# Performance work log

Hardware: AMD Instinct MI355X
Metric: run time of the kernel (lower is better)

Reference implementation:

```python
import jax, jax.numpy as jnp
import numpy as np

B = 32768
IN_DIM = 256
HIDDEN = 256  # max(64, in_dim)
E = 8         # num_size_classes
K = 5         # num_depth_classes


def setup_inputs() -> dict:
    key = jax.random.key(0)
    ks = jax.random.split(key, 6)
    x = jax.random.normal(ks[0], (B, IN_DIM), dtype=jnp.float32)
    size_idx = jax.random.randint(ks[1], (B,), 0, E, dtype=jnp.int32)
    s1 = 1.0 / np.sqrt(IN_DIM)
    s2 = 1.0 / np.sqrt(HIDDEN)
    W1 = jax.random.uniform(ks[2], (E, IN_DIM, HIDDEN), jnp.float32, -s1, s1)
    b1 = jax.random.uniform(ks[3], (E, HIDDEN), jnp.float32, -s1, s1)
    W2 = jax.random.uniform(ks[4], (E, HIDDEN, K - 1), jnp.float32, -s2, s2)
    b2 = jax.random.uniform(ks[5], (E, K - 1), jnp.float32, -s2, s2)
    return {"x": x, "size_idx": size_idx, "W1": W1, "b1": b1, "W2": W2, "b2": b2}


def ordinal_logits_to_probs(logits):
    # logits: [B, K-1] cumulative ordinal logits -> [B, K] class probabilities
    q = jax.nn.sigmoid(logits)
    probs = jnp.concatenate(
        [1.0 - q[:, :1], q[:, :-1] - q[:, 1:], q[:, -1:]], axis=1)
    probs = jnp.clip(probs, 1e-8)
    return probs / jnp.clip(jnp.sum(probs, axis=1, keepdims=True), 1e-8)


def reference(x, size_idx, W1, b1, W2, b2):
    # Hard expert dispatch: each sample routed to expert[size_idx].
    # Equivalent to torch's boolean-mask loop (every row has a valid expert).
    # Compute all experts densely (grouped GEMM), then select per sample.
    h = jax.nn.relu(jnp.einsum('bi,eih->beh', x, W1) + b1)       # [B,E,H]
    logits_all = jnp.einsum('beh,ehk->bek', h, W2) + b2           # [B,E,K-1]
    idx = size_idx.astype(jnp.int32)[:, None, None]               # [B,1,1]
    logits = jnp.take_along_axis(logits_all, idx, axis=1)[:, 0]   # [B,K-1]
    probs = ordinal_logits_to_probs(logits)
    return logits, probs
```

## Files before the change

### kernel.cpp

```cpp
#include <hip/hip_runtime.h>
#include <stdint.h>
#include <math.h>

#define B_N   32768
#define INDIM 256
#define HID   256
#define NE    8
#define KM1   4
#define KCLS  5
#define BM    64
#define CAP   8192
#define TPE   (CAP / BM)
#define NBLK  (NE * TPE)

typedef __bf16 bf16x8 __attribute__((ext_vector_type(8)));
typedef float  f32x4  __attribute__((ext_vector_type(4)));
typedef unsigned short u16x8 __attribute__((ext_vector_type(8)));

__device__ __forceinline__ unsigned short f2bf(float f) {
    union { float f; unsigned u; } v; v.f = f;
    unsigned r = v.u + 0x7FFFu + ((v.u >> 16) & 1u);
    return (unsigned short)(r >> 16);
}
__device__ __forceinline__ float bf2f(unsigned short b) {
    union { unsigned u; float f; } v; v.u = ((unsigned)b) << 16;
    return v.f;
}
__device__ __forceinline__ int SWZ(int r, int c) { return c ^ (r & 7); }

__device__ __forceinline__ void gload_lds16(const void* g, void* l) {
    __builtin_amdgcn_global_load_lds(
        (__attribute__((address_space(1))) unsigned int*)(g),
        (__attribute__((address_space(3))) unsigned int*)(l),
        16, 0, 0);
}

__global__ __launch_bounds__(256) void k_w1t(const float* __restrict__ W1,
                                             const int* __restrict__ sidx,
                                             unsigned short* __restrict__ w1p,
                                             int* __restrict__ part) {
    __shared__ float tile[64][65];
    __shared__ int wc[4][NE];
    int t    = threadIdx.x;
    int b    = blockIdx.x;
    int lane = t & 63;
    int wave = t >> 6;

    int es = sidx[b * 256 + t];
    #pragma unroll
    for (int t2 = 0; t2 < NE; ++t2) {
        unsigned long long m = __ballot(es == t2);
        if (lane == t2) wc[wave][t2] = (int)__popcll(m);
    }

    int e  = b >> 4, ti = (b >> 2) & 3, th = b & 3;
    const float* src = W1 + (((size_t)e * INDIM) + (size_t)ti * 64) * HID + th * 64;
    int col = t & 63, r0 = (t >> 6) * 16;
    #pragma unroll
    for (int rr = 0; rr < 16; ++rr)
        tile[r0 + rr][col] = src[(size_t)(r0 + rr) * HID + col];
    __syncthreads();

    if (t < NE) {
        part[(2 * b) * NE + t]     = wc[0][t] + wc[1][t];
        part[(2 * b + 1) * NE + t] = wc[2][t] + wc[3][t];
    }

    int u = t >> 6;
    #pragma unroll
    for (int ks2 = 0; ks2 < 2; ++ks2) {
        int ks = ti * 2 + ks2, nb = th * 4 + u;
        u16x8 v;
        #pragma unroll
        for (int j = 0; j < 8; ++j)
            v[j] = f2bf(tile[ks2 * 32 + (lane >> 4) * 8 + j][u * 16 + (lane & 15)]);
        *(u16x8*)&w1p[((((size_t)e * 8 + ks) * 16 + nb) * 64 + lane) * 8] = v;
    }
}

__global__ __launch_bounds__(256) void k_xscat(
    const float* __restrict__ x, const int* __restrict__ sidx,
    const int* __restrict__ part,
    unsigned short* __restrict__ xb, int* __restrict__ perm,
    int* __restrict__ meta)
{
    __shared__ int pp[256][NE];
    __shared__ int pr[8][NE][2];
    __shared__ int pre8[NE], tot8[NE];
    __shared__ int wc0[NE];
    __shared__ int posbuf[128];

    int t    = threadIdx.x;
    int b    = blockIdx.x;
    int lane = t & 63;
    int wave = t >> 6;

    #pragma unroll
    for (int e2 = 0; e2 < NE; ++e2) pp[t][e2] = part[t * NE + e2];

    int e_own = 0, posw = 0;
    if (t < 128) {
        e_own = sidx[b * 128 + t];
        #pragma unroll
        for (int t2 = 0; t2 < NE; ++t2) {
            unsigned long long m = __ballot(e_own == t2);
            if (e_own == t2) posw = (int)__popcll(m & ((1ull << lane) - 1ull));
            if (wave == 0 && lane == t2) wc0[t2] = (int)__popcll(m);
        }
    }
    __syncthreads();

    if (t < 64) {
        int e2 = t & 7, r = t >> 3;
        int sb = 0, sa = 0;
        #pragma unroll
        for (int c = 0; c < 32; ++c) {
            int ch = r * 32 + c;
            int v  = pp[ch][e2];
            sb += (ch < b) ? v : 0;
            sa += v;
        }
        pr[r][e2][0] = sb; pr[r][e2][1] = sa;
    }
    __syncthreads();
    if (t < NE) {
        int sb = 0, sa = 0;
        #pragma unroll
        for (int r = 0; r < 8; ++r) { sb += pr[r][t][0]; sa += pr[r][t][1]; }
        pre8[t] = sb; tot8[t] = sa;
        meta[t] = sa;
    }
    __syncthreads();

    if (t < 128) {
        int rank = pre8[e_own] + ((wave == 1) ? wc0[e_own] : 0) + posw;
        int pos  = e_own * CAP + rank;
        posbuf[t] = pos;
        perm[pos] = b * 128 + t;
    }
    __syncthreads();

    {
        int si  = t & 127, h = t >> 7;
        int pos = posbuf[si];
        int r   = pos & (BM - 1);
        const float* xr = x + (size_t)(b * 128 + si) * INDIM + h * 128;
        unsigned short* dst = xb + (size_t)pos * 256;
        #pragma unroll
        for (int cc = 0; cc < 16; ++cc) {
            int ch   = h * 16 + cc;
            int slot = SWZ(r, ch);
            f32x4 a0 = *(const f32x4*)(xr + cc * 8);
            f32x4 a1 = *(const f32x4*)(xr + cc * 8 + 4);
            u16x8 v;
            v[0] = f2bf(a0[0]); v[1] = f2bf(a0[1]); v[2] = f2bf(a0[2]); v[3] = f2bf(a0[3]);
            v[4] = f2bf(a1[0]); v[5] = f2bf(a1[1]); v[6] = f2bf(a1[2]); v[7] = f2bf(a1[3]);
            *(u16x8*)&dst[slot * 8] = v;
        }
    }
}

__global__ __launch_bounds__(256, 4) void k_main(
    const float* __restrict__ b1, const float* __restrict__ W2,
    const float* __restrict__ b2,
    const unsigned short* __restrict__ w1p,
    const unsigned short* __restrict__ xb,
    const int* __restrict__ perm, const int* __restrict__ meta,
    float* __restrict__ out)
{
    __shared__ unsigned short xs[BM * 256];
    __shared__ float w2s[1040];

    int bid = (blockIdx.x & 7) * TPE + (blockIdx.x >> 3);
    int e   = bid >> 7;
    int tl  = bid & (TPE - 1);
    int cnt = meta[e];
    int rb  = tl * BM;
    if (rb >= cnt) return;
    int segc = cnt - rb;

    int tid  = threadIdx.x;
    int lane = tid & 63;
    int wave = tid >> 6;
    int r15  = lane & 15;
    int hi   = lane >> 4;

    const unsigned short* xbt = xb + ((size_t)e * CAP + rb) * 256;
    #pragma unroll
    for (int it = 0; it < 8; ++it)
        gload_lds16(xbt + ((size_t)it * 256 + tid) * 8, &xs[it * 2048 + wave * 512]);

    const unsigned short* w1pe = w1p + (size_t)e * (8 * 16 * 64 * 8);
    auto loadB = [&](int ks, int ni) -> bf16x8 {
        return *(const bf16x8*)&w1pe[(((ks * 16 + wave * 4 + ni) * 64) + lane) * 8];
    };
    bf16x8 bcur[4];
    #pragma unroll
    for (int ni = 0; ni < 4; ++ni) bcur[ni] = loadB(0, ni);

    {
        const float* w2e = W2 + (size_t)e * HID * KM1;
        f32x4 wv = *(const f32x4*)(w2e + (size_t)tid * 4);
        *(f32x4*)&w2s[tid * 4 + (tid >> 6) * 4] = wv;
    }
    __syncthreads();

    f32x4 acc[4][4];
    #pragma unroll
    for (int mi = 0; mi < 4; ++mi)
        #pragma unroll
        for (int ni = 0; ni < 4; ++ni) {
            f32x4 z = {0.f, 0.f, 0.f, 0.f};
            acc[mi][ni] = z;
        }

    #pragma unroll
    for (int ks = 0; ks < 8; ++ks) {
        bf16x8 bnext[4];
        if (ks < 7) {
            #pragma unroll
            for (int ni = 0; ni < 4; ++ni) bnext[ni] = loadB(ks + 1, ni);
        }
        bf16x8 af[4];
        #pragma unroll
        for (int mi = 0; mi < 4; ++mi) {
            int r = mi * 16 + r15;
            af[mi] = *(const bf16x8*)&xs[r * 256 + (SWZ(r, ks * 4 + hi) << 3)];
        }
        #pragma unroll
        for (int mi = 0; mi < 4; ++mi)
            #pragma unroll
            for (int ni = 0; ni < 4; ++ni)
                acc[mi][ni] = __builtin_amdgcn_mfma_f32_16x16x32_bf16(
                    af[mi], bcur[ni], acc[mi][ni], 0, 0, 0);
        if (ks < 7) {
            #pragma unroll
            for (int ni = 0; ni < 4; ++ni) bcur[ni] = bnext[ni];
        }
    }
    __syncthreads();

    float b1v[4];
    #pragma unroll
    for (int ni = 0; ni < 4; ++ni)
        b1v[ni] = b1[e * HID + wave * 64 + ni * 16 + r15];
    #pragma unroll
    for (int mi = 0; mi < 4; ++mi) {
        #pragma unroll
        for (int ni = 0; ni < 4; ++ni) {
            int colg  = wave * 64 + ni * 16 + r15;
            int chunk = colg >> 3;
            #pragma unroll
            for (int j = 0; j < 4; ++j) {
                int rowg = mi * 16 + hi * 4 + j;
                float h = fmaxf(acc[mi][ni][j] + b1v[ni], 0.f);
                xs[rowg * 256 + (SWZ(rowg, chunk) << 3) + (colg & 7)] = f2bf(h);
            }
        }
    }
    __syncthreads();

    int row = tid >> 2;
    int q   = tid & 3;
    f32x4 lac = {0.f, 0.f, 0.f, 0.f};
    #pragma unroll
    for (int s = 0; s < 8; ++s) {
        int c = q * 8 + s;
        u16x8 hv = *(const u16x8*)&xs[row * 256 + (SWZ(row, c) << 3)];
        #pragma unroll
        for (int j = 0; j < 8; ++j) {
            int k = c * 8 + j;
            float hf = bf2f(hv[j]);
            const f32x4 wv = *(const f32x4*)&w2s[k * 4 + (k >> 6) * 4];
            lac[0] += hf * wv[0]; lac[1] += hf * wv[1];
            lac[2] += hf * wv[2]; lac[3] += hf * wv[3];
        }
    }
    #pragma unroll
    for (int c4 = 0; c4 < 4; ++c4) {
        lac[c4] += __shfl_xor(lac[c4], 1, 4);
        lac[c4] += __shfl_xor(lac[c4], 2, 4);
    }

    if (row < segc) {
        int smp = perm[(size_t)e * CAP + rb + row];
        const float* b2e = b2 + e * KM1;
        float l0 = lac[0] + b2e[0], l1 = lac[1] + b2e[1];
        float l2 = lac[2] + b2e[2], l3 = lac[3] + b2e[3];
        float q0 = 1.f / (1.f + expf(-l0)), q1 = 1.f / (1.f + expf(-l1));
        float q2v = 1.f / (1.f + expf(-l2)), q3 = 1.f / (1.f + expf(-l3));
        float p0 = fmaxf(1.f - q0, 1e-8f), p1 = fmaxf(q0 - q1, 1e-8f);
        float p2 = fmaxf(q1 - q2v, 1e-8f), p3 = fmaxf(q2v - q3, 1e-8f);
        float p4 = fmaxf(q3, 1e-8f);
        float inv = 1.f / (p0 + p1 + p2 + p3 + p4);
        float myl = (q & 1) ? ((q & 2) ? l3 : l1) : ((q & 2) ? l2 : l0);
        float myp = (q & 1) ? ((q & 2) ? p3 : p1) : ((q & 2) ? p2 : p0);
        out[(size_t)smp * KM1 + q] = myl;
        float* probs = out + (size_t)B_N * KM1;
        probs[(size_t)smp * KCLS + q] = myp * inv;
        if (q == 3) probs[(size_t)smp * KCLS + 4] = p4 * inv;
    }
}

extern "C" void kernel_launch(void* const* d_in, const int* in_sizes, int n_in,
                              void* d_out, int out_size, void* d_ws, size_t ws_size,
                              hipStream_t stream) {
    const float* x   = (const float*)d_in[0];
    const int*   sid = (const int*)d_in[1];
    const float* W1  = (const float*)d_in[2];
    const float* b1  = (const float*)d_in[3];
    const float* W2  = (const float*)d_in[4];
    const float* b2  = (const float*)d_in[5];
    float* out = (float*)d_out;

    char* ws = (char*)d_ws;
    unsigned short* w1p = (unsigned short*)ws;
    unsigned short* xb  = (unsigned short*)(ws + 1048576);
    int* perm = (int*)(ws + 1048576 + 33554432);
    int* part = (int*)(ws + 1048576 + 33554432 + 262144);
    int* meta = (int*)(ws + 1048576 + 33554432 + 262144 + 8192);

    k_w1t  <<<dim3(128),  dim3(256), 0, stream>>>(W1, sid, w1p, part);
    k_xscat<<<dim3(256),  dim3(256), 0, stream>>>(x, sid, part, xb, perm, meta);
    k_main <<<dim3(NBLK), dim3(256), 0, stream>>>(b1, W2, b2, w1p, xb, perm, meta, out);
}
```

Measured before the change: 42.19 us.

## Split scatter kernel into rank computation and wide x-to-bf16 conversion kernel

Splits the combined rank-and-scatter kernel into two kernels. k_rank computes each sample's destination position and writes it to a new pos buffer. k_xconv then converts x to bf16 and scatters it using 2048 blocks, with 16 threads per row, instead of 256 blocks where each thread walked half a row. The aim is more parallelism and memory-level concurrency for the bandwidth-bound conversion. It also transposes the shared partition array to cut LDS bank conflicts. The cost is an extra kernel launch and a round trip of the pos buffer through global memory.

```diff
diff --git a/kernel.cpp b/kernel.cpp
--- a/kernel.cpp
+++ b/kernel.cpp
@@ -78,17 +78,13 @@
     }
 }
 
-__global__ __launch_bounds__(256) void k_xscat(
-    const float* __restrict__ x, const int* __restrict__ sidx,
-    const int* __restrict__ part,
-    unsigned short* __restrict__ xb, int* __restrict__ perm,
-    int* __restrict__ meta)
+__global__ __launch_bounds__(256) void k_rank(
+    const int* __restrict__ sidx, const int* __restrict__ part,
+    int* __restrict__ pos, int* __restrict__ perm, int* __restrict__ meta)
 {
-    __shared__ int pp[256][NE];
+    __shared__ int pp[NE][260];
     __shared__ int pr[8][NE][2];
-    __shared__ int pre8[NE], tot8[NE];
-    __shared__ int wc0[NE];
-    __shared__ int posbuf[128];
+    __shared__ int pre8[NE], tot8[NE], wc0[NE];
 
     int t    = threadIdx.x;
     int b    = blockIdx.x;
@@ -96,7 +92,7 @@
     int wave = t >> 6;
 
     #pragma unroll
-    for (int e2 = 0; e2 < NE; ++e2) pp[t][e2] = part[t * NE + e2];
+    for (int e2 = 0; e2 < NE; ++e2) pp[e2][t] = part[t * NE + e2];
 
     int e_own = 0, posw = 0;
     if (t < 128) {
@@ -116,7 +112,7 @@
         #pragma unroll
         for (int c = 0; c < 32; ++c) {
             int ch = r * 32 + c;
-            int v  = pp[ch][e2];
+            int v  = pp[e2][ch];
             sb += (ch < b) ? v : 0;
             sa += v;
         }
@@ -134,29 +130,33 @@
 
     if (t < 128) {
         int rank = pre8[e_own] + ((wave == 1) ? wc0[e_own] : 0) + posw;
-        int pos  = e_own * CAP + rank;
-        posbuf[t] = pos;
-        perm[pos] = b * 128 + t;
-    }
-    __syncthreads();
-
-    {
-        int si  = t & 127, h = t >> 7;
-        int pos = posbuf[si];
-        int r   = pos & (BM - 1);
-        const float* xr = x + (size_t)(b * 128 + si) * INDIM + h * 128;
-        unsigned short* dst = xb + (size_t)pos * 256;
-        #pragma unroll
-        for (int cc = 0; cc < 16; ++cc) {
-            int ch   = h * 16 + cc;
-            int slot = SWZ(r, ch);
-            f32x4 a0 = *(const f32x4*)(xr + cc * 8);
-            f32x4 a1 = *(const f32x4*)(xr + cc * 8 + 4);
-            u16x8 v;
-            v[0] = f2bf(a0[0]); v[1] = f2bf(a0[1]); v[2] = f2bf(a0[2]); v[3] = f2bf(a0[3]);
-            v[4] = f2bf(a1[0]); v[5] = f2bf(a1[1]); v[6] = f2bf(a1[2]); v[7] = f2bf(a1[3]);
-            *(u16x8*)&dst[slot * 8] = v;
-        }
+        int p    = e_own * CAP + rank;
+        pos[b * 128 + t] = p;
+        perm[p] = b * 128 + t;
+    }
+}
+
+__global__ __launch_bounds__(256) void k_xconv(
+    const float* __restrict__ x, const int* __restrict__ pos,
+    unsigned short* __restrict__ xb)
+{
+    int g    = blockIdx.x;
+    int rloc = threadIdx.x >> 4;
+    int p    = threadIdx.x & 15;
+    int smp  = g * 16 + rloc;
+    int ps   = pos[smp];
+    int r    = ps & (BM - 1);
+    const float* xr = x + (size_t)smp * INDIM + p * 16;
+    unsigned short* dst = xb + (size_t)ps * 256;
+    #pragma unroll
+    for (int cc = 0; cc < 2; ++cc) {
+        int ch = p * 2 + cc;
+        f32x4 a0 = *(const f32x4*)(xr + cc * 8);
+        f32x4 a1 = *(const f32x4*)(xr + cc * 8 + 4);
+        u16x8 v;
+        v[0] = f2bf(a0[0]); v[1] = f2bf(a0[1]); v[2] = f2bf(a0[2]); v[3] = f2bf(a0[3]);
+        v[4] = f2bf(a1[0]); v[5] = f2bf(a1[1]); v[6] = f2bf(a1[2]); v[7] = f2bf(a1[3]);
+        *(u16x8*)&dst[SWZ(r, ch) * 8] = v;
     }
 }
 
@@ -316,11 +316,13 @@
     char* ws = (char*)d_ws;
     unsigned short* w1p = (unsigned short*)ws;
     unsigned short* xb  = (unsigned short*)(ws + 1048576);
-    int* perm = (int*)(ws + 1048576 + 33554432);
-    int* part = (int*)(ws + 1048576 + 33554432 + 262144);
-    int* meta = (int*)(ws + 1048576 + 33554432 + 262144 + 8192);
+    int* perm = (int*)(ws + 34603008);
+    int* part = (int*)(ws + 34865152);
+    int* meta = (int*)(ws + 34873344);
+    int* pos  = (int*)(ws + 34873600);
 
     k_w1t  <<<dim3(128),  dim3(256), 0, stream>>>(W1, sid, w1p, part);
-    k_xscat<<<dim3(256),  dim3(256), 0, stream>>>(x, sid, part, xb, perm, meta);
+    k_rank <<<dim3(256),  dim3(256), 0, stream>>>(sid, part, pos, perm, meta);
+    k_xconv<<<dim3(2048), dim3(256), 0, stream>>>(x, pos, xb);
     k_main <<<dim3(NBLK), dim3(256), 0, stream>>>(b1, W2, b2, w1p, xb, perm, meta, out);
 }
```

After: 39.03 us. -7.5%, faster.

## Fuse W1 transpose and x scatter into one kernel with grid-wide atomic barrier

Applied to the files above, without the earlier changes.

Merges the W1 bf16 packing kernel and the x scatter/permutation kernel into a single 256-block kernel. Per-block expert counts are published through release atomics and a global done counter, and each block spins until all blocks have arrived before computing prefix offsets. This removes one kernel launch and its inter-kernel gap, but adds a memset launch and a spin barrier. The barrier depends on all 256 blocks being resident at the same time.

```diff
diff --git a/kernel.cpp b/kernel.cpp
--- a/kernel.cpp
+++ b/kernel.cpp
@@ -10,6 +10,8 @@
 #define KCLS  5
 #define BM    64
 #define CAP   8192
+#define GRID_P 256
+#define SPB   128
 #define TPE   (CAP / BM)
 #define NBLK  (NE * TPE)
 
@@ -35,78 +37,76 @@
         16, 0, 0);
 }
 
-__global__ __launch_bounds__(256) void k_w1t(const float* __restrict__ W1,
-                                             const int* __restrict__ sidx,
-                                             unsigned short* __restrict__ w1p,
-                                             int* __restrict__ part) {
+__global__ __launch_bounds__(256) void k_prep(
+    const float* __restrict__ W1, const float* __restrict__ x,
+    const int* __restrict__ sidx,
+    unsigned short* __restrict__ w1p, unsigned short* __restrict__ xb,
+    int* __restrict__ perm, int* __restrict__ wpart,
+    int* __restrict__ meta, int* __restrict__ done)
+{
     __shared__ float tile[64][65];
-    __shared__ int wc[4][NE];
+    __shared__ int   pp[NE][260];
+    __shared__ int   pr[8][NE][2];
+    __shared__ int   pre8[NE], tot8[NE];
+    __shared__ int   wc01[2][NE];
+    __shared__ int   posbuf[SPB];
+
     int t    = threadIdx.x;
-    int b    = blockIdx.x;
+    int blk  = blockIdx.x;
     int lane = t & 63;
     int wave = t >> 6;
 
-    int es = sidx[b * 256 + t];
-    #pragma unroll
-    for (int t2 = 0; t2 < NE; ++t2) {
-        unsigned long long m = __ballot(es == t2);
-        if (lane == t2) wc[wave][t2] = (int)__popcll(m);
-    }
-
-    int e  = b >> 4, ti = (b >> 2) & 3, th = b & 3;
-    const float* src = W1 + (((size_t)e * INDIM) + (size_t)ti * 64) * HID + th * 64;
-    int col = t & 63, r0 = (t >> 6) * 16;
-    #pragma unroll
-    for (int rr = 0; rr < 16; ++rr)
-        tile[r0 + rr][col] = src[(size_t)(r0 + rr) * HID + col];
-    __syncthreads();
-
-    if (t < NE) {
-        part[(2 * b) * NE + t]     = wc[0][t] + wc[1][t];
-        part[(2 * b + 1) * NE + t] = wc[2][t] + wc[3][t];
-    }
-
-    int u = t >> 6;
-    #pragma unroll
-    for (int ks2 = 0; ks2 < 2; ++ks2) {
-        int ks = ti * 2 + ks2, nb = th * 4 + u;
-        u16x8 v;
-        #pragma unroll
-        for (int j = 0; j < 8; ++j)
-            v[j] = f2bf(tile[ks2 * 32 + (lane >> 4) * 8 + j][u * 16 + (lane & 15)]);
-        *(u16x8*)&w1p[((((size_t)e * 8 + ks) * 16 + nb) * 64 + lane) * 8] = v;
-    }
-}
-
-__global__ __launch_bounds__(256) void k_xscat(
-    const float* __restrict__ x, const int* __restrict__ sidx,
-    const int* __restrict__ part,
-    unsigned short* __restrict__ xb, int* __restrict__ perm,
-    int* __restrict__ meta)
-{
-    __shared__ int pp[256][NE];
-    __shared__ int pr[8][NE][2];
-    __shared__ int pre8[NE], tot8[NE];
-    __shared__ int wc0[NE];
-    __shared__ int posbuf[128];
-
-    int t    = threadIdx.x;
-    int b    = blockIdx.x;
-    int lane = t & 63;
-    int wave = t >> 6;
-
-    #pragma unroll
-    for (int e2 = 0; e2 < NE; ++e2) pp[t][e2] = part[t * NE + e2];
-
-    int e_own = 0, posw = 0;
-    if (t < 128) {
-        e_own = sidx[b * 128 + t];
+    int mye = -1, posw = 0;
+    if (t < SPB) {
+        mye = sidx[blk * SPB + t];
         #pragma unroll
         for (int t2 = 0; t2 < NE; ++t2) {
-            unsigned long long m = __ballot(e_own == t2);
-            if (e_own == t2) posw = (int)__popcll(m & ((1ull << lane) - 1ull));
-            if (wave == 0 && lane == t2) wc0[t2] = (int)__popcll(m);
-        }
+            unsigned long long m = __ballot(mye == t2);
+            if (mye == t2) posw = (int)__popcll(m & ((1ull << lane) - 1ull));
+            if (lane == t2) wc01[wave][t2] = (int)__popcll(m);
+        }
+    }
+    __syncthreads();
+
+    if (t < NE)
+        __hip_atomic_store(&wpart[blk * NE + t], wc01[0][t] + wc01[1][t],
+                           __ATOMIC_RELEASE, __HIP_MEMORY_SCOPE_AGENT);
+    __syncthreads();
+    if (t == 0)
+        __hip_atomic_fetch_add(done, 1, __ATOMIC_RELEASE, __HIP_MEMORY_SCOPE_AGENT);
+
+    if (blk < 128) {
+        int e = blk >> 4, ti = (blk >> 2) & 3, th = blk & 3;
+        const float* src = W1 + (((size_t)e * INDIM) + (size_t)ti * 64) * HID + th * 64;
+        int col = t & 63, r0 = (t >> 6) * 16;
+        #pragma unroll
+        for (int rr = 0; rr < 16; ++rr)
+            tile[r0 + rr][col] = src[(size_t)(r0 + rr) * HID + col];
+        __syncthreads();
+        int u = t >> 6;
+        #pragma unroll
+        for (int ks2 = 0; ks2 < 2; ++ks2) {
+            int ks = ti * 2 + ks2, nb = th * 4 + u;
+            u16x8 v;
+            #pragma unroll
+            for (int j = 0; j < 8; ++j)
+                v[j] = f2bf(tile[ks2 * 32 + (lane >> 4) * 8 + j][u * 16 + (lane & 15)]);
+            *(u16x8*)&w1p[((((size_t)e * 8 + ks) * 16 + nb) * 64 + lane) * 8] = v;
+        }
+    }
+
+    if (t == 0) {
+        while (__hip_atomic_load(done, __ATOMIC_ACQUIRE,
+                                 __HIP_MEMORY_SCOPE_AGENT) < GRID_P)
+            __builtin_amdgcn_s_sleep(2);
+    }
+    __syncthreads();
+
+    {
+        #pragma unroll
+        for (int i = 0; i < NE; ++i)
+            pp[i][t] = __hip_atomic_load(&wpart[t * NE + i], __ATOMIC_RELAXED,
+                                         __HIP_MEMORY_SCOPE_AGENT);
     }
     __syncthreads();
 
@@ -116,9 +116,8 @@
         #pragma unroll
         for (int c = 0; c < 32; ++c) {
             int ch = r * 32 + c;
-            int v  = pp[ch][e2];
-            sb += (ch < b) ? v : 0;
-            sa += v;
+            int v  = pp[e2][ch];
+            sa += v; sb += (ch < blk) ? v : 0;
         }
         pr[r][e2][0] = sb; pr[r][e2][1] = sa;
     }
@@ -132,11 +131,11 @@
     }
     __syncthreads();
 
-    if (t < 128) {
-        int rank = pre8[e_own] + ((wave == 1) ? wc0[e_own] : 0) + posw;
-        int pos  = e_own * CAP + rank;
+    if (t < SPB) {
+        int rank = pre8[mye] + ((wave == 1) ? wc01[0][mye] : 0) + posw;
+        int pos  = mye * CAP + rank;
         posbuf[t] = pos;
-        perm[pos] = b * 128 + t;
+        perm[pos] = blk * SPB + t;
     }
     __syncthreads();
 
@@ -144,18 +143,17 @@
         int si  = t & 127, h = t >> 7;
         int pos = posbuf[si];
         int r   = pos & (BM - 1);
-        const float* xr = x + (size_t)(b * 128 + si) * INDIM + h * 128;
+        const float* xr = x + (size_t)(blk * SPB + si) * INDIM + h * 128;
         unsigned short* dst = xb + (size_t)pos * 256;
         #pragma unroll
         for (int cc = 0; cc < 16; ++cc) {
-            int ch   = h * 16 + cc;
-            int slot = SWZ(r, ch);
+            int ch = h * 16 + cc;
             f32x4 a0 = *(const f32x4*)(xr + cc * 8);
             f32x4 a1 = *(const f32x4*)(xr + cc * 8 + 4);
             u16x8 v;
             v[0] = f2bf(a0[0]); v[1] = f2bf(a0[1]); v[2] = f2bf(a0[2]); v[3] = f2bf(a0[3]);
             v[4] = f2bf(a1[0]); v[5] = f2bf(a1[1]); v[6] = f2bf(a1[2]); v[7] = f2bf(a1[3]);
-            *(u16x8*)&dst[slot * 8] = v;
+            *(u16x8*)&dst[SWZ(r, ch) * 8] = v;
         }
     }
 }
@@ -260,8 +258,7 @@
     }
     __syncthreads();
 
-    int row = tid >> 2;
-    int q   = tid & 3;
+    int row = tid >> 2, q = tid & 3;
     f32x4 lac = {0.f, 0.f, 0.f, 0.f};
     #pragma unroll
     for (int s = 0; s < 8; ++s) {
@@ -277,9 +274,9 @@
         }
     }
     #pragma unroll
-    for (int c4 = 0; c4 < 4; ++c4) {
-        lac[c4] += __shfl_xor(lac[c4], 1, 4);
-        lac[c4] += __shfl_xor(lac[c4], 2, 4);
+    for (int c4_ = 0; c4_ < 4; ++c4_) {
+        lac[c4_] += __shfl_xor(lac[c4_], 1, 4);
+        lac[c4_] += __shfl_xor(lac[c4_], 2, 4);
     }
 
     if (row < segc) {
@@ -287,11 +284,11 @@
         const float* b2e = b2 + e * KM1;
         float l0 = lac[0] + b2e[0], l1 = lac[1] + b2e[1];
         float l2 = lac[2] + b2e[2], l3 = lac[3] + b2e[3];
-        float q0 = 1.f / (1.f + expf(-l0)), q1 = 1.f / (1.f + expf(-l1));
-        float q2v = 1.f / (1.f + expf(-l2)), q3 = 1.f / (1.f + expf(-l3));
-        float p0 = fmaxf(1.f - q0, 1e-8f), p1 = fmaxf(q0 - q1, 1e-8f);
-        float p2 = fmaxf(q1 - q2v, 1e-8f), p3 = fmaxf(q2v - q3, 1e-8f);
-        float p4 = fmaxf(q3, 1e-8f);
+        float q0 = 1.f / (1.f + expf(-l0)), q1v = 1.f / (1.f + expf(-l1));
+        float q2v = 1.f / (1.f + expf(-l2)), q3v = 1.f / (1.f + expf(-l3));
+        float p0 = fmaxf(1.f - q0, 1e-8f), p1 = fmaxf(q0 - q1v, 1e-8f);
+        float p2 = fmaxf(q1v - q2v, 1e-8f), p3 = fmaxf(q2v - q3v, 1e-8f);
+        float p4 = fmaxf(q3v, 1e-8f);
         float inv = 1.f / (p0 + p1 + p2 + p3 + p4);
         float myl = (q & 1) ? ((q & 2) ? l3 : l1) : ((q & 2) ? l2 : l0);
         float myp = (q & 1) ? ((q & 2) ? p3 : p1) : ((q & 2) ? p2 : p0);
@@ -316,11 +313,14 @@
     char* ws = (char*)d_ws;
     unsigned short* w1p = (unsigned short*)ws;
     unsigned short* xb  = (unsigned short*)(ws + 1048576);
-    int* perm = (int*)(ws + 1048576 + 33554432);
-    int* part = (int*)(ws + 1048576 + 33554432 + 262144);
-    int* meta = (int*)(ws + 1048576 + 33554432 + 262144 + 8192);
-
-    k_w1t  <<<dim3(128),  dim3(256), 0, stream>>>(W1, sid, w1p, part);
-    k_xscat<<<dim3(256),  dim3(256), 0, stream>>>(x, sid, part, xb, perm, meta);
-    k_main <<<dim3(NBLK), dim3(256), 0, stream>>>(b1, W2, b2, w1p, xb, perm, meta, out);
-}
+    int* perm  = (int*)(ws + 34603008);
+    int* wpart = (int*)(ws + 34865152);
+    int* meta  = (int*)(ws + 34873600);
+    int* done  = (int*)(ws + 34873664);
+
+    hipMemsetAsync(done, 0, 4, stream);
+    k_prep<<<dim3(GRID_P), dim3(256), 0, stream>>>(W1, x, sid, w1p, xb,
+                                                   perm, wpart, meta, done);
+    k_main<<<dim3(NBLK),   dim3(256), 0, stream>>>(b1, W2, b2, w1p, xb,
+                                                   perm, meta, out);
+}
```

Result: slower. 57.54 us (+36.4%).
